# Optimization experiments

Hardware: AMD Instinct MI355X
Metric: run time of the kernel (lower is better)

Reference implementation:

```python
import jax, jax.numpy as jnp
import numpy as np
import math

DIM = 1024
WINDOW = 16
NUM_HEADS = 16
HEAD_DIM = DIM // NUM_HEADS
SCALE = math.sqrt(HEAD_DIM)
LN_EPS = 1e-5


def _gather_window(z, W):
    # z: [B, T, H, C] -> [B, T, H, W, C]; nb[:, t, :, w, :] = z[:, t-1-w] (zeros if t-1-w < 0)
    B, T, H, C = z.shape
    t = jnp.arange(T)[:, None]
    w = jnp.arange(W)[None, :]
    idx = t - 1 - w                      # [T, W]
    valid = idx >= 0
    idxc = jnp.clip(idx, 0, T - 1)
    nb = z[:, idxc]                      # [B, T, W, H, C]
    nb = jnp.where(valid[None, :, :, None, None], nb, jnp.zeros((), z.dtype))
    return nb.transpose(0, 1, 3, 2, 4)   # [B, T, H, W, C]


def setup_inputs() -> dict:
    key = jax.random.key(0)
    k0, k1, k2, k3 = jax.random.split(key, 4)
    B, T, D = 2, 4096, DIM
    x = jax.random.normal(k0, (B, T, D), dtype=jnp.float32)
    wq = jax.random.normal(k1, (D, D), dtype=jnp.float32) * 0.02
    wkv = jax.random.normal(k2, (2 * D, D), dtype=jnp.float32) * 0.02  # torch Linear weight layout [out,in]
    wo = jax.random.normal(k3, (D, D), dtype=jnp.float32) * 0.02
    gamma = jnp.ones((D,), dtype=jnp.float32)
    beta = jnp.zeros((D,), dtype=jnp.float32)
    return {"x": x, "wq": wq, "wkv": wkv, "wo": wo, "gamma": gamma, "beta": beta}


def reference(x, wq, wkv, wo, gamma, beta):
    B, T, D = x.shape
    H, HD, W = NUM_HEADS, HEAD_DIM, WINDOW
    q = (x @ wq.T).reshape(B, T, H, HD)
    kv = (x @ wkv.T).reshape(B, T, H, 2 * HD)
    nb_kv = _gather_window(kv, W)                    # [B, T, H, W, 2*HD]
    nb_k, nb_v = nb_kv[..., :HD], nb_kv[..., HD:]
    tau = jax.nn.sigmoid(jnp.einsum('bthd,bthwd->bthw', q, nb_k) / SCALE)
    msg = jnp.einsum('bthw,bthwd->bthd', tau, nb_v)  # [B, T, H, HD]
    y = x + msg.reshape(B, T, D) @ wo.T
    mu = jnp.mean(y, axis=-1, keepdims=True)
    var = jnp.mean((y - mu) ** 2, axis=-1, keepdims=True)
    out = (y - mu) * jax.lax.rsqrt(var + LN_EPS) * gamma + beta
    return out
```

## Files before the change

kernel.cpp:

```cpp
#include <hip/hip_runtime.h>
#include <hip/hip_bf16.h>

#define D_MODEL 1024
#define SEQ_T   4096
#define NBATCH  2
#define NHEADS  16
#define HEAD_D  64
#define WIN     16

typedef __attribute__((ext_vector_type(8))) short bf16x8;
typedef __attribute__((ext_vector_type(8))) unsigned short u16x8;
typedef __attribute__((ext_vector_type(4))) float f32x4;

__device__ __forceinline__ unsigned short f2bf(float f) {
  union { float f; unsigned int u; } v; v.f = f;
  unsigned int r = v.u + 0x7fffu + ((v.u >> 16) & 1u);
  return (unsigned short)(r >> 16);
}
__device__ __forceinline__ float bf2f(unsigned short u) {
  union { unsigned int u; float f; } v; v.u = ((unsigned int)u) << 16;
  return v.f;
}

#define SBAR() __builtin_amdgcn_s_barrier()
#define LGKM0() asm volatile("s_waitcnt lgkmcnt(0)" ::: "memory")
#define LGKM8() asm volatile("s_waitcnt lgkmcnt(8)" ::: "memory")
#define VMC(n) asm volatile("s_waitcnt vmcnt(" #n ")" ::: "memory")

__global__ __launch_bounds__(256) void cast_all(const float4* __restrict__ x,
                                                const float4* __restrict__ wq,
                                                const float4* __restrict__ wkv,
                                                const float4* __restrict__ wo,
                                                ushort* __restrict__ xb,
                                                ushort* __restrict__ wb) {
  int i = blockIdx.x * 256 + threadIdx.x;
  float4 v;
  ushort* dst;
  if (i < 2097152) {
    v = x[i];
    dst = xb + (size_t)i * 4;
  } else {
    int j = i - 2097152;
    const float4* src;
    int off;
    if (j < 262144) { src = wq; off = 0; }
    else if (j < 786432) { src = wkv; off = 262144; }
    else { src = wo; off = 786432; }
    v = src[j - off];
    dst = wb + (size_t)j * 4;
  }
  ushort4 o;
  o.x = f2bf(v.x); o.y = f2bf(v.y); o.z = f2bf(v.z); o.w = f2bf(v.w);
  *(ushort4*)dst = o;
}

__global__ __launch_bounds__(256, 2) void gemm1_2pc(const ushort* __restrict__ A,
                                                    const ushort* __restrict__ Bt,
                                                    ushort* __restrict__ C,
                                                    int M, int N, int K) {
  extern __shared__ char smem[];
  const int NTK = K >> 6;
  const int tid = threadIdx.x;
  const int wid = tid >> 6;
  const int lane = tid & 63;
  const int lin = blockIdx.y * 16 + blockIdx.x;
  const int swz = (lin & 7) * 128 + (lin >> 3);
  const int m0 = (swz >> 4) * 128;
  const int n0 = (swz & 15) * 192;

  const int l8 = lane >> 3;
  const int lchunk = (lane & 7) ^ (l8 & 7);
  const ushort* pA = A + (size_t)(m0 + wid * 8 + l8) * K + lchunk * 8;
  const ushort* pB = Bt + (size_t)(n0 + wid * 8 + l8) * K + lchunk * 8;

#define SA(kt, db)                                                                         \
  {                                                                                        \
    _Pragma("unroll") for (int j = 0; j < 4; ++j) {                                        \
      const ushort* gp = pA + (size_t)(j * 32) * K + (size_t)(kt) * 64;                    \
      char* lp = smem + (db) * 16384 + (j * 4 + wid) * 1024;                               \
      __builtin_amdgcn_global_load_lds((const __attribute__((address_space(1))) void*)gp,  \
                                       (__attribute__((address_space(3))) void*)lp, 16, 0, 0); \
    }                                                                                      \
  }
#define SB(kt, db, j0)                                                                     \
  {                                                                                        \
    _Pragma("unroll") for (int j = (j0); j < (j0) + 3; ++j) {                              \
      const ushort* gp = pB + (size_t)(j * 32) * K + (size_t)(kt) * 64;                    \
      char* lp = smem + 32768 + (db) * 24576 + (j * 4 + wid) * 1024;                       \
      __builtin_amdgcn_global_load_lds((const __attribute__((address_space(1))) void*)gp,  \
                                       (__attribute__((address_space(3))) void*)lp, 16, 0, 0); \
    }                                                                                      \
  }

  const int fr = lane & 15;
  const int g = lane >> 4;
  const int wr = wid >> 1;
  const int wc = wid & 1;
  int aRow[4], bRow[6], ch[2];
#pragma unroll
  for (int mi = 0; mi < 4; ++mi) aRow[mi] = (wr * 64 + mi * 16 + fr) * 128;
#pragma unroll
  for (int j = 0; j < 6; ++j) bRow[j] = (wc * 96 + j * 16 + fr) * 128;
#pragma unroll
  for (int kk = 0; kk < 2; ++kk) ch[kk] = ((kk * 4 + g) ^ (fr & 7)) * 16;

  f32x4 acc[4][6];
#pragma unroll
  for (int mi = 0; mi < 4; ++mi)
#pragma unroll
    for (int j = 0; j < 6; ++j) acc[mi][j] = (f32x4){0.f, 0.f, 0.f, 0.f};

  bf16x8 a[4][2], b[2][2];

#define RD_A(db)                                                               \
  _Pragma("unroll") for (int mi = 0; mi < 4; ++mi)                             \
    _Pragma("unroll") for (int kk = 0; kk < 2; ++kk)                           \
      a[mi][kk] = *(const bf16x8*)(smem + (db) * 16384 + aRow[mi] + ch[kk]);
#define RD_B(db, nh)                                                           \
  _Pragma("unroll") for (int ni = 0; ni < 2; ++ni)                             \
    _Pragma("unroll") for (int kk = 0; kk < 2; ++kk)                           \
      b[ni][kk] = *(const bf16x8*)(smem + 32768 + (db) * 24576 +               \
                                   bRow[(nh) * 2 + ni] + ch[kk]);
#define MM(nh)                                                                 \
  __builtin_amdgcn_s_setprio(1);                                               \
  _Pragma("unroll") for (int kk = 0; kk < 2; ++kk)                             \
    _Pragma("unroll") for (int mi = 0; mi < 4; ++mi)                           \
      _Pragma("unroll") for (int ni = 0; ni < 2; ++ni)                         \
        acc[mi][(nh) * 2 + ni] = __builtin_amdgcn_mfma_f32_16x16x32_bf16(      \
            a[mi][kk], b[ni][kk], acc[mi][(nh) * 2 + ni], 0, 0, 0);            \
  __builtin_amdgcn_s_setprio(0);

  SA(0, 0); SB(0, 0, 0); SB(0, 0, 3); SA(1, 1);
  VMC(4);
  SBAR();

#pragma unroll 1
  for (int t = 0; t < NTK; ++t) {
    const int db = t & 1;
    const int t1 = (t + 1 < NTK) ? t + 1 : NTK - 1;
    const int t2 = (t + 2 < NTK) ? t + 2 : NTK - 1;
    const int d1 = t1 & 1, d2 = t2 & 1;

    RD_A(db); RD_B(db, 0);
    SB(t1, d1, 0);
    LGKM8();
    SBAR(); LGKM0();
    MM(0);
    SBAR();

    RD_B(db, 1);
    SB(t1, d1, 3);
    SBAR(); LGKM0();
    MM(1);
    SBAR();

    RD_B(db, 2);
    SA(t2, d2);
    VMC(4);
    SBAR(); LGKM0();
    MM(2);
    SBAR();
  }

  const int cc = lane & 15;
  const int cr4 = (lane >> 4) * 4;
#pragma unroll
  for (int mi = 0; mi < 4; ++mi)
#pragma unroll
    for (int j = 0; j < 6; ++j)
#pragma unroll
      for (int r = 0; r < 4; ++r) {
        int row = m0 + wr * 64 + mi * 16 + cr4 + r;
        int col = n0 + wc * 96 + j * 16 + cc;
        C[(size_t)row * N + col] = f2bf(acc[mi][j][r]);
      }
#undef SA
#undef SB
#undef RD_A
#undef RD_B
#undef MM
}

__global__ __launch_bounds__(512, 2) void gemm2_b(const ushort* __restrict__ A,
                                                  const ushort* __restrict__ Bt,
                                                  const ushort* __restrict__ residb,
                                                  ushort* __restrict__ Yb,
                                                  int M, int N, int K) {
  extern __shared__ char smem[];
  const int NTK = K >> 6;
  const int tid = threadIdx.x;
  const int wid = tid >> 6;
  const int lane = tid & 63;
  const int lin = blockIdx.y * 8 + blockIdx.x;
  const int swz = (lin & 7) * 32 + (lin >> 3);
  const int m0 = (swz >> 3) * 256;
  const int n0 = (swz & 7) * 128;

  const int l8 = lane >> 3;
  const int lchunk = (lane & 7) ^ (l8 & 7);
  const ushort* pA = A + (size_t)(m0 + wid * 8 + l8) * K + lchunk * 8;
  const ushort* pB = Bt + (size_t)(n0 + wid * 8 + l8) * K + lchunk * 8;

#define STAGE_A(kt, db)                                                                    \
  {                                                                                        \
    _Pragma("unroll") for (int j = 0; j < 4; ++j) {                                        \
      const ushort* gp = pA + (size_t)(j * 64) * K + (size_t)(kt) * 64;                    \
      char* lp = smem + (db) * 32768 + (j * 8 + wid) * 1024;                               \
      __builtin_amdgcn_global_load_lds((const __attribute__((address_space(1))) void*)gp,  \
                                       (__attribute__((address_space(3))) void*)lp, 16, 0, 0); \
    }                                                                                      \
  }
#define STAGE_B(kt, db)                                                                    \
  {                                                                                        \
    _Pragma("unroll") for (int j = 0; j < 2; ++j) {                                        \
      const ushort* gp = pB + (size_t)(j * 64) * K + (size_t)(kt) * 64;                    \
      char* lp = smem + 65536 + (db) * 16384 + (j * 8 + wid) * 1024;                       \
      __builtin_amdgcn_global_load_lds((const __attribute__((address_space(1))) void*)gp,  \
                                       (__attribute__((address_space(3))) void*)lp, 16, 0, 0); \
    }                                                                                      \
  }

  const int fr = lane & 15;
  const int g = lane >> 4;
  const int wr = wid >> 1;
  const int wc = wid & 1;
  int aRow[4], bRow[2][2], ch[2];
#pragma unroll
  for (int mi = 0; mi < 4; ++mi) aRow[mi] = (wr * 64 + mi * 16 + fr) * 128;
#pragma unroll
  for (int nq = 0; nq < 2; ++nq)
#pragma unroll
    for (int ni = 0; ni < 2; ++ni) bRow[nq][ni] = (wc * 64 + nq * 32 + ni * 16 + fr) * 128;
#pragma unroll
  for (int kk = 0; kk < 2; ++kk) ch[kk] = ((kk * 4 + g) ^ (fr & 7)) * 16;

  f32x4 acc[2][4][2];
#pragma unroll
  for (int nq = 0; nq < 2; ++nq)
#pragma unroll
    for (int mi = 0; mi < 4; ++mi)
#pragma unroll
      for (int ni = 0; ni < 2; ++ni) acc[nq][mi][ni] = (f32x4){0.f, 0.f, 0.f, 0.f};

  bf16x8 a[4][2], b0[2][2], b1[2][2];

  STAGE_A(0, 0); STAGE_B(0, 0); STAGE_A(1, 1);
  VMC(4);
  SBAR();

#define PHASE_MFMA(nq, bfr)                                                    \
  __builtin_amdgcn_s_setprio(1);                                               \
  _Pragma("unroll") for (int kk = 0; kk < 2; ++kk)                             \
    _Pragma("unroll") for (int mi = 0; mi < 4; ++mi)                           \
      _Pragma("unroll") for (int ni = 0; ni < 2; ++ni)                         \
        acc[nq][mi][ni] = __builtin_amdgcn_mfma_f32_16x16x32_bf16(             \
            a[mi][kk], bfr[ni][kk], acc[nq][mi][ni], 0, 0, 0);                 \
  __builtin_amdgcn_s_setprio(0);

#pragma unroll 1
  for (int t = 0; t < NTK; ++t) {
    const int db = t & 1;
    const int u1 = (t + 1 < NTK) ? t + 1 : NTK - 1;
    const int u2 = (t + 2 < NTK) ? t + 2 : NTK - 1;
    const int d1 = u1 & 1, d2 = u2 & 1;
    const char* Ab = smem + db * 32768;
    const char* Bb = smem + 65536 + db * 16384;

#pragma unroll
    for (int mi = 0; mi < 4; ++mi)
#pragma unroll
      for (int kk = 0; kk < 2; ++kk)
        a[mi][kk] = *(const bf16x8*)(Ab + aRow[mi] + ch[kk]);
#pragma unroll
    for (int ni = 0; ni < 2; ++ni)
#pragma unroll
      for (int kk = 0; kk < 2; ++kk)
        b0[ni][kk] = *(const bf16x8*)(Bb + bRow[0][ni] + ch[kk]);
    STAGE_B(u1, d1);
    LGKM0();
    PHASE_MFMA(0, b0);
    VMC(2);
    SBAR();

#pragma unroll
    for (int ni = 0; ni < 2; ++ni)
#pragma unroll
      for (int kk = 0; kk < 2; ++kk)
        b1[ni][kk] = *(const bf16x8*)(Bb + bRow[1][ni] + ch[kk]);
    STAGE_A(u2, d2);
    LGKM0();
    PHASE_MFMA(1, b1);
    VMC(4);
    SBAR();
  }

  const int cc = lane & 15;
  const int cr4 = (lane >> 4) * 4;
#pragma unroll
  for (int nq = 0; nq < 2; ++nq)
#pragma unroll
    for (int mi = 0; mi < 4; ++mi)
#pragma unroll
      for (int ni = 0; ni < 2; ++ni)
#pragma unroll
        for (int r = 0; r < 4; ++r) {
          int row = m0 + wr * 64 + mi * 16 + cr4 + r;
          int col = n0 + wc * 64 + nq * 32 + ni * 16 + cc;
          size_t idx = (size_t)row * N + col;
          Yb[idx] = f2bf(acc[nq][mi][ni][r] + bf2f(residb[idx]));
        }
#undef STAGE_A
#undef STAGE_B
#undef PHASE_MFMA
}

__global__ __launch_bounds__(256) void attn_win_mfma(const ushort* __restrict__ qkv,
                                                     ushort* __restrict__ msg) {
  __shared__ ushort Ks[80][72];
  __shared__ ushort Vt[64][88];
  __shared__ ushort Ps[4][16][40];

  const int tile = blockIdx.x;
  const int h = blockIdx.y;
  const int b = blockIdx.z;
  const int t0 = tile * 64;
  const size_t rowbase = (size_t)b * SEQ_T;
  const int tid = threadIdx.x;
  const int wave = tid >> 6;
  const int lane = tid & 63;

  for (int chunk = tid; chunk < 1280; chunk += 256) {
    int r = chunk >> 4;
    int c = (chunk & 15) * 8;
    int t = t0 - 16 + r;
    u16x8 u = {0, 0, 0, 0, 0, 0, 0, 0};
    if (t >= 0)
      u = *(const u16x8*)(qkv + (rowbase + t) * 3072 + 1024 + (size_t)h * 128 + c);
    if (c < 64) {
      *(u16x8*)&Ks[r][c] = u;
    } else {
      int d0 = c - 64;
#pragma unroll
      for (int j = 0; j < 8; ++j) Vt[d0 + j][r] = u[j];
    }
  }
  __syncthreads();

  const int fr = lane & 15;
  const int g = lane >> 4;
  const int rbase = wave * 16;

  bf16x8 qa[2];
#pragma unroll
  for (int kk = 0; kk < 2; ++kk)
    qa[kk] = *(const bf16x8*)(qkv + (rowbase + t0 + wave * 16 + fr) * 3072 +
                              (size_t)h * 64 + kk * 32 + g * 8);

  f32x4 sacc[2];
  sacc[0] = (f32x4){0.f, 0.f, 0.f, 0.f};
  sacc[1] = (f32x4){0.f, 0.f, 0.f, 0.f};
#pragma unroll
  for (int kk = 0; kk < 2; ++kk) {
#pragma unroll
    for (int nt = 0; nt < 2; ++nt) {
      bf16x8 kb = *(const bf16x8*)&Ks[rbase + nt * 16 + fr][kk * 32 + g * 8];
      sacc[nt] = __builtin_amdgcn_mfma_f32_16x16x32_bf16(qa[kk], kb, sacc[nt], 0, 0, 0);
    }
  }

#pragma unroll
  for (int nt = 0; nt < 2; ++nt) {
    int tk = t0 - 16 + rbase + nt * 16 + fr;
#pragma unroll
    for (int reg = 0; reg < 4; ++reg) {
      int t = t0 + wave * 16 + g * 4 + reg;
      float tau = 0.f;
      if (tk >= 0 && tk >= t - WIN && tk <= t - 1)
        tau = 1.f / (1.f + __expf(-sacc[nt][reg] * 0.125f));
      Ps[wave][g * 4 + reg][nt * 16 + fr] = f2bf(tau);
    }
  }
  __syncthreads();

  bf16x8 pa = *(const bf16x8*)&Ps[wave][fr][g * 8];
#pragma unroll
  for (int ct = 0; ct < 4; ++ct) {
    bf16x8 vb = *(const bf16x8*)&Vt[ct * 16 + fr][rbase + g * 8];
    f32x4 m = __builtin_amdgcn_mfma_f32_16x16x32_bf16(pa, vb, (f32x4){0.f, 0.f, 0.f, 0.f}, 0, 0, 0);
#pragma unroll
    for (int reg = 0; reg < 4; ++reg) {
      int t = t0 + wave * 16 + g * 4 + reg;
      msg[(rowbase + t) * 1024 + (size_t)h * 64 + ct * 16 + fr] = f2bf(m[reg]);
    }
  }
}

__global__ __launch_bounds__(256) void layernorm_b(const ushort* __restrict__ yb,
                                                   const float* __restrict__ gamma,
                                                   const float* __restrict__ beta,
                                                   float* __restrict__ out) {
  const int row = blockIdx.x;
  const ushort* p = yb + (size_t)row * D_MODEL;
  const int tid = threadIdx.x;
  ushort4 v4 = ((const ushort4*)p)[tid];
  float y0 = bf2f(v4.x), y1 = bf2f(v4.y), y2 = bf2f(v4.z), y3 = bf2f(v4.w);
  float s = y0 + y1 + y2 + y3;
  float s2 = y0 * y0 + y1 * y1 + y2 * y2 + y3 * y3;
#pragma unroll
  for (int m = 1; m < 64; m <<= 1) {
    s += __shfl_xor(s, m);
    s2 += __shfl_xor(s2, m);
  }
  __shared__ float red[8];
  const int wave = tid >> 6, lane = tid & 63;
  if (lane == 0) { red[wave] = s; red[4 + wave] = s2; }
  __syncthreads();
  s = red[0] + red[1] + red[2] + red[3];
  s2 = red[4] + red[5] + red[6] + red[7];
  const float mu = s * (1.f / D_MODEL);
  const float var = s2 * (1.f / D_MODEL) - mu * mu;
  const float rstd = rsqrtf(var + 1e-5f);
  float4 g = *(const float4*)&gamma[tid * 4];
  float4 be = *(const float4*)&beta[tid * 4];
  float4 o;
  o.x = (y0 - mu) * rstd * g.x + be.x;
  o.y = (y1 - mu) * rstd * g.y + be.y;
  o.z = (y2 - mu) * rstd * g.z + be.z;
  o.w = (y3 - mu) * rstd * g.w + be.w;
  *(float4*)&out[(size_t)row * D_MODEL + tid * 4] = o;
}

extern "C" void kernel_launch(void* const* d_in, const int* in_sizes, int n_in,
                              void* d_out, int out_size, void* d_ws, size_t ws_size,
                              hipStream_t stream) {
  (void)in_sizes; (void)n_in; (void)out_size; (void)ws_size;
  const float* x = (const float*)d_in[0];
  const float* wq = (const float*)d_in[1];
  const float* wkv = (const float*)d_in[2];
  const float* wo = (const float*)d_in[3];
  const float* gamma = (const float*)d_in[4];
  const float* beta = (const float*)d_in[5];
  float* out = (float*)d_out;

  ushort* xb = (ushort*)d_ws;
  ushort* wb = xb + (size_t)8192 * 1024;
  ushort* qkvb = wb + (size_t)4096 * 1024;
  ushort* msgb = qkvb + (size_t)8192 * 3072;
  ushort* yb = qkvb;

  const int M = NBATCH * SEQ_T;

  (void)hipFuncSetAttribute(reinterpret_cast<const void*>(&gemm1_2pc),
                            hipFuncAttributeMaxDynamicSharedMemorySize, 81920);
  (void)hipFuncSetAttribute(reinterpret_cast<const void*>(&gemm2_b),
                            hipFuncAttributeMaxDynamicSharedMemorySize, 98304);

  cast_all<<<12288, 256, 0, stream>>>((const float4*)x, (const float4*)wq,
                                      (const float4*)wkv, (const float4*)wo, xb, wb);

  gemm1_2pc<<<dim3(3072 / 192, M / 128), 256, 81920, stream>>>(xb, wb, qkvb, M, 3072, 1024);

  attn_win_mfma<<<dim3(SEQ_T / 64, NHEADS, NBATCH), 256, 0, stream>>>(qkvb, msgb);

  gemm2_b<<<dim3(1024 / 128, M / 256), 512, 98304, stream>>>(msgb, wb + (size_t)3072 * 1024,
                                                             xb, yb, M, 1024, 1024);

  layernorm_b<<<M, 256, 0, stream>>>(yb, gamma, beta, out);
}
```

Baseline: 117.3 us.

## Shrink output-projection GEMM tile to 128x128 with 4-wave blocks

The second GEMM (msg @ wo^T plus residual) now uses 128x128 tiles with 256 threads instead of 256x128 tiles with 512 threads. This doubles the grid to 512 blocks and cuts LDS use to 64KB, so more blocks can be resident per CU on an 8192x1024 problem. The k-loop schedule also changes: each half-step now places a barrier before its MFMA phase and waits on LDS reads differently. In exchange, each block reuses its A and B tiles less, and the extra barriers add synchronisation.

```diff
diff --git a/kernel.cpp b/kernel.cpp
--- a/kernel.cpp
+++ b/kernel.cpp
@@ -181,19 +181,19 @@
 #undef MM
 }
 
-__global__ __launch_bounds__(512, 2) void gemm2_b(const ushort* __restrict__ A,
-                                                  const ushort* __restrict__ Bt,
-                                                  const ushort* __restrict__ residb,
-                                                  ushort* __restrict__ Yb,
-                                                  int M, int N, int K) {
+__global__ __launch_bounds__(256, 2) void gemm2_2pc(const ushort* __restrict__ A,
+                                                    const ushort* __restrict__ Bt,
+                                                    const ushort* __restrict__ residb,
+                                                    ushort* __restrict__ Yb,
+                                                    int M, int N, int K) {
   extern __shared__ char smem[];
   const int NTK = K >> 6;
   const int tid = threadIdx.x;
   const int wid = tid >> 6;
   const int lane = tid & 63;
   const int lin = blockIdx.y * 8 + blockIdx.x;
-  const int swz = (lin & 7) * 32 + (lin >> 3);
-  const int m0 = (swz >> 3) * 256;
+  const int swz = (lin & 7) * 64 + (lin >> 3);
+  const int m0 = (swz >> 3) * 128;
   const int n0 = (swz & 7) * 128;
 
   const int l8 = lane >> 3;
@@ -201,20 +201,20 @@
   const ushort* pA = A + (size_t)(m0 + wid * 8 + l8) * K + lchunk * 8;
   const ushort* pB = Bt + (size_t)(n0 + wid * 8 + l8) * K + lchunk * 8;
 
-#define STAGE_A(kt, db)                                                                    \
+#define SA2(kt, db)                                                                        \
   {                                                                                        \
     _Pragma("unroll") for (int j = 0; j < 4; ++j) {                                        \
-      const ushort* gp = pA + (size_t)(j * 64) * K + (size_t)(kt) * 64;                    \
-      char* lp = smem + (db) * 32768 + (j * 8 + wid) * 1024;                               \
+      const ushort* gp = pA + (size_t)(j * 32) * K + (size_t)(kt) * 64;                    \
+      char* lp = smem + (db) * 16384 + (j * 4 + wid) * 1024;                               \
       __builtin_amdgcn_global_load_lds((const __attribute__((address_space(1))) void*)gp,  \
                                        (__attribute__((address_space(3))) void*)lp, 16, 0, 0); \
     }                                                                                      \
   }
-#define STAGE_B(kt, db)                                                                    \
+#define SB2(kt, db)                                                                        \
   {                                                                                        \
-    _Pragma("unroll") for (int j = 0; j < 2; ++j) {                                        \
-      const ushort* gp = pB + (size_t)(j * 64) * K + (size_t)(kt) * 64;                    \
-      char* lp = smem + 65536 + (db) * 16384 + (j * 8 + wid) * 1024;                       \
+    _Pragma("unroll") for (int j = 0; j < 4; ++j) {                                        \
+      const ushort* gp = pB + (size_t)(j * 32) * K + (size_t)(kt) * 64;                    \
+      char* lp = smem + 32768 + (db) * 16384 + (j * 4 + wid) * 1024;                       \
       __builtin_amdgcn_global_load_lds((const __attribute__((address_space(1))) void*)gp,  \
                                        (__attribute__((address_space(3))) void*)lp, 16, 0, 0); \
     }                                                                                      \
@@ -224,94 +224,84 @@
   const int g = lane >> 4;
   const int wr = wid >> 1;
   const int wc = wid & 1;
-  int aRow[4], bRow[2][2], ch[2];
+  int aRow[4], bRow[4], ch[2];
 #pragma unroll
   for (int mi = 0; mi < 4; ++mi) aRow[mi] = (wr * 64 + mi * 16 + fr) * 128;
 #pragma unroll
-  for (int nq = 0; nq < 2; ++nq)
-#pragma unroll
-    for (int ni = 0; ni < 2; ++ni) bRow[nq][ni] = (wc * 64 + nq * 32 + ni * 16 + fr) * 128;
+  for (int j = 0; j < 4; ++j) bRow[j] = (wc * 64 + j * 16 + fr) * 128;
 #pragma unroll
   for (int kk = 0; kk < 2; ++kk) ch[kk] = ((kk * 4 + g) ^ (fr & 7)) * 16;
 
-  f32x4 acc[2][4][2];
-#pragma unroll
-  for (int nq = 0; nq < 2; ++nq)
-#pragma unroll
-    for (int mi = 0; mi < 4; ++mi)
-#pragma unroll
-      for (int ni = 0; ni < 2; ++ni) acc[nq][mi][ni] = (f32x4){0.f, 0.f, 0.f, 0.f};
-
-  bf16x8 a[4][2], b0[2][2], b1[2][2];
-
-  STAGE_A(0, 0); STAGE_B(0, 0); STAGE_A(1, 1);
-  VMC(4);
-  SBAR();
-
-#define PHASE_MFMA(nq, bfr)                                                    \
+  f32x4 acc[4][4];
+#pragma unroll
+  for (int mi = 0; mi < 4; ++mi)
+#pragma unroll
+    for (int j = 0; j < 4; ++j) acc[mi][j] = (f32x4){0.f, 0.f, 0.f, 0.f};
+
+  bf16x8 a[4][2], b[2][2];
+
+#define RD_A2(db)                                                              \
+  _Pragma("unroll") for (int mi = 0; mi < 4; ++mi)                             \
+    _Pragma("unroll") for (int kk = 0; kk < 2; ++kk)                           \
+      a[mi][kk] = *(const bf16x8*)(smem + (db) * 16384 + aRow[mi] + ch[kk]);
+#define RD_B2(db, nh)                                                          \
+  _Pragma("unroll") for (int ni = 0; ni < 2; ++ni)                             \
+    _Pragma("unroll") for (int kk = 0; kk < 2; ++kk)                           \
+      b[ni][kk] = *(const bf16x8*)(smem + 32768 + (db) * 16384 +               \
+                                   bRow[(nh) * 2 + ni] + ch[kk]);
+#define MM2(nh)                                                                \
   __builtin_amdgcn_s_setprio(1);                                               \
   _Pragma("unroll") for (int kk = 0; kk < 2; ++kk)                             \
     _Pragma("unroll") for (int mi = 0; mi < 4; ++mi)                           \
       _Pragma("unroll") for (int ni = 0; ni < 2; ++ni)                         \
-        acc[nq][mi][ni] = __builtin_amdgcn_mfma_f32_16x16x32_bf16(             \
-            a[mi][kk], bfr[ni][kk], acc[nq][mi][ni], 0, 0, 0);                 \
+        acc[mi][(nh) * 2 + ni] = __builtin_amdgcn_mfma_f32_16x16x32_bf16(      \
+            a[mi][kk], b[ni][kk], acc[mi][(nh) * 2 + ni], 0, 0, 0);            \
   __builtin_amdgcn_s_setprio(0);
+
+  SA2(0, 0); SB2(0, 0); SA2(1, 1);
+  VMC(4);
+  SBAR();
 
 #pragma unroll 1
   for (int t = 0; t < NTK; ++t) {
     const int db = t & 1;
-    const int u1 = (t + 1 < NTK) ? t + 1 : NTK - 1;
-    const int u2 = (t + 2 < NTK) ? t + 2 : NTK - 1;
-    const int d1 = u1 & 1, d2 = u2 & 1;
-    const char* Ab = smem + db * 32768;
-    const char* Bb = smem + 65536 + db * 16384;
-
-#pragma unroll
-    for (int mi = 0; mi < 4; ++mi)
-#pragma unroll
-      for (int kk = 0; kk < 2; ++kk)
-        a[mi][kk] = *(const bf16x8*)(Ab + aRow[mi] + ch[kk]);
-#pragma unroll
-    for (int ni = 0; ni < 2; ++ni)
-#pragma unroll
-      for (int kk = 0; kk < 2; ++kk)
-        b0[ni][kk] = *(const bf16x8*)(Bb + bRow[0][ni] + ch[kk]);
-    STAGE_B(u1, d1);
-    LGKM0();
-    PHASE_MFMA(0, b0);
-    VMC(2);
+    const int t1 = (t + 1 < NTK) ? t + 1 : NTK - 1;
+    const int t2 = (t + 2 < NTK) ? t + 2 : NTK - 1;
+    const int d1 = t1 & 1, d2 = t2 & 1;
+
+    RD_A2(db); RD_B2(db, 0);
+    SB2(t1, d1);
+    LGKM8();
+    SBAR(); LGKM0();
+    MM2(0);
     SBAR();
 
-#pragma unroll
-    for (int ni = 0; ni < 2; ++ni)
-#pragma unroll
-      for (int kk = 0; kk < 2; ++kk)
-        b1[ni][kk] = *(const bf16x8*)(Bb + bRow[1][ni] + ch[kk]);
-    STAGE_A(u2, d2);
-    LGKM0();
-    PHASE_MFMA(1, b1);
+    RD_B2(db, 1);
+    SA2(t2, d2);
     VMC(4);
+    SBAR(); LGKM0();
+    MM2(1);
     SBAR();
   }
 
   const int cc = lane & 15;
   const int cr4 = (lane >> 4) * 4;
 #pragma unroll
-  for (int nq = 0; nq < 2; ++nq)
-#pragma unroll
-    for (int mi = 0; mi < 4; ++mi)
-#pragma unroll
-      for (int ni = 0; ni < 2; ++ni)
-#pragma unroll
-        for (int r = 0; r < 4; ++r) {
-          int row = m0 + wr * 64 + mi * 16 + cr4 + r;
-          int col = n0 + wc * 64 + nq * 32 + ni * 16 + cc;
-          size_t idx = (size_t)row * N + col;
-          Yb[idx] = f2bf(acc[nq][mi][ni][r] + bf2f(residb[idx]));
-        }
-#undef STAGE_A
-#undef STAGE_B
-#undef PHASE_MFMA
+  for (int mi = 0; mi < 4; ++mi)
+#pragma unroll
+    for (int j = 0; j < 4; ++j)
+#pragma unroll
+      for (int r = 0; r < 4; ++r) {
+        int row = m0 + wr * 64 + mi * 16 + cr4 + r;
+        int col = n0 + wc * 64 + j * 16 + cc;
+        size_t idx = (size_t)row * N + col;
+        Yb[idx] = f2bf(acc[mi][j][r] + bf2f(residb[idx]));
+      }
+#undef SA2
+#undef SB2
+#undef RD_A2
+#undef RD_B2
+#undef MM2
 }
 
 __global__ __launch_bounds__(256) void attn_win_mfma(const ushort* __restrict__ qkv,
@@ -452,8 +442,8 @@
 
   (void)hipFuncSetAttribute(reinterpret_cast<const void*>(&gemm1_2pc),
                             hipFuncAttributeMaxDynamicSharedMemorySize, 81920);
-  (void)hipFuncSetAttribute(reinterpret_cast<const void*>(&gemm2_b),
-                            hipFuncAttributeMaxDynamicSharedMemorySize, 98304);
+  (void)hipFuncSetAttribute(reinterpret_cast<const void*>(&gemm2_2pc),
+                            hipFuncAttributeMaxDynamicSharedMemorySize, 65536);
 
   cast_all<<<12288, 256, 0, stream>>>((const float4*)x, (const float4*)wq,
                                       (const float4*)wkv, (const float4*)wo, xb, wb);
@@ -462,8 +452,8 @@
 
   attn_win_mfma<<<dim3(SEQ_T / 64, NHEADS, NBATCH), 256, 0, stream>>>(qkvb, msgb);
 
-  gemm2_b<<<dim3(1024 / 128, M / 256), 512, 98304, stream>>>(msgb, wb + (size_t)3072 * 1024,
-                                                             xb, yb, M, 1024, 1024);
+  gemm2_2pc<<<dim3(1024 / 128, M / 128), 256, 65536, stream>>>(msgb, wb + (size_t)3072 * 1024,
+                                                               xb, yb, M, 1024, 1024);
 
   layernorm_b<<<M, 256, 0, stream>>>(yb, gamma, beta, out);
 }
```

Measured after the change: 116.2 us (median of 2 runs). No clear change (-1.0%).
